# Optimization experiments

Measured on AMD Instinct MI355X. Metric: run time of the kernel, lower is better.

The kernel has to match this reference:

```python
import jax, jax.numpy as jnp
import numpy as np

S, B, D, Z, C, H = 256, 1024, 64, 32, 64, 128
L = 2 * S + 3  # len(ext_ts); _xs[0::2][1:-1] must match xs -> L = 2*S+3


def setup_inputs() -> dict:
    key = jax.random.key(0)
    ks = jax.random.split(key, 16)

    def xavier(k, out_d, in_d):
        lim = float(np.sqrt(6.0 / (in_d + out_d)))
        return jax.random.uniform(k, (out_d, in_d), minval=-lim, maxval=lim, dtype=jnp.float32)

    bias = lambda n: jnp.full((n,), 0.01, jnp.float32)  # m.bias.data.fill_(0.01)

    return {
        "xs": jax.random.normal(ks[0], (S, B, D), jnp.float32),
        "ext_ts": jnp.arange(L, dtype=jnp.float32) * 0.01,  # spacing <= dt=0.02 -> 1 euler step/interval
        "eps_z0": jax.random.normal(ks[1], (B, Z), jnp.float32),
        "dW": jax.random.normal(ks[2], (L - 1, B, Z), jnp.float32),  # standard normal; scaled by sqrt(dt) inside
        "gru_Wih": xavier(ks[3], 3 * H, D),
        "gru_Whh": xavier(ks[4], 3 * H, H),
        "gru_bih": jnp.zeros((3 * H,), jnp.float32),
        "gru_bhh": jnp.zeros((3 * H,), jnp.float32),
        "enc_W": xavier(ks[5], C, H), "enc_b": bias(C),
        "qz0_W": xavier(ks[6], 2 * Z, C), "qz0_b": bias(2 * Z),
        "f_W1": xavier(ks[7], H, Z + 1), "f_b1": bias(H),
        "f_W2": xavier(ks[8], H, H), "f_b2": bias(H),
        "f_W3": xavier(ks[9], Z, H), "f_b3": bias(Z),
        "g_W1": xavier(ks[10], H, Z + 1), "g_b1": bias(H),
        "g_W2": xavier(ks[11], Z, H), "g_b2": bias(Z),
        "proj_W": xavier(ks[12], D, Z), "proj_b": bias(D),
        "pz0_mean": jnp.zeros((1, Z), jnp.float32),
        "pz0_logstd": jnp.zeros((1, Z), jnp.float32),
    }


def reference(xs, ext_ts, eps_z0, dW, gru_Wih, gru_Whh, gru_bih, gru_bhh,
              enc_W, enc_b, qz0_W, qz0_b,
              f_W1, f_b1, f_W2, f_b2, f_W3, f_b3,
              g_W1, g_b1, g_W2, g_b2,
              proj_W, proj_b, pz0_mean, pz0_logstd):
    nb = xs.shape[1]
    # ---- Encoder: GRU over time-reversed xs; only ctx[0] (after flip-back) is
    # used, which equals lin(final hidden of the reversed-sequence GRU).
    x_rev = xs[::-1]
    gi_all = jnp.einsum('sbd,hd->sbh', x_rev, gru_Wih) + gru_bih  # (S,B,3H)

    def gru_step(h, gi_t):
        gh = h @ gru_Whh.T + gru_bhh
        i_r, i_z, i_n = jnp.split(gi_t, 3, axis=-1)
        h_r, h_z, h_n = jnp.split(gh, 3, axis=-1)
        r = jax.nn.sigmoid(i_r + h_r)
        zg = jax.nn.sigmoid(i_z + h_z)
        n = jnp.tanh(i_n + r * h_n)
        return (1.0 - zg) * n + zg * h, None

    hT, _ = jax.lax.scan(gru_step, jnp.zeros((nb, gru_Whh.shape[1]), xs.dtype), gi_all)
    ctx0 = hT @ enc_W.T + enc_b

    # ---- q(z0) and reparameterized sample
    q = ctx0 @ qz0_W.T + qz0_b
    qz0_mean, qz0_logstd = jnp.split(q, 2, axis=1)
    z0 = qz0_mean + jnp.exp(qz0_logstd) * eps_z0

    # ---- Euler-Maruyama SDE integration (diagonal noise), one step per interval
    dts = ext_ts[1:] - ext_ts[:-1]

    def sde_step(z, inp):
        t, dt, dw = inp
        tcol = jnp.broadcast_to(t.reshape(1, 1), (z.shape[0], 1)).astype(z.dtype)
        tz = jnp.concatenate([tcol, z], axis=1)  # (B, Z+1)
        h1 = jax.nn.relu(tz @ f_W1.T + f_b1)
        h2 = jax.nn.relu(h1 @ f_W2.T + f_b2)
        drift = h2 @ f_W3.T + f_b3
        gh = jax.nn.relu(tz @ g_W1.T + g_b1)
        diff = gh @ g_W2.T + g_b2
        z_new = z + drift * dt + diff * (jnp.sqrt(dt) * dw)
        return z_new, z_new

    _, zs_rest = jax.lax.scan(sde_step, z0, (ext_ts[:-1], dts, dW))
    zs = jnp.concatenate([z0[None], zs_rest], axis=0)  # (L,B,Z)

    # ---- project to data space and compute losses
    xs_hat = jnp.einsum('lbz,dz->lbd', zs, proj_W) + proj_b
    recon_xs = xs_hat[0::2][1:-1]   # (S,B,D)
    interp_xs = xs_hat[1::2][1:-1]  # (S-1,B,D)
    recon_loss = jnp.mean((recon_xs - xs) ** 2)

    # KL( N(qm, e^qls) || N(pm, e^pls) ), summed over latent, averaged over batch
    kl = (pz0_logstd - qz0_logstd
          + (jnp.exp(2.0 * qz0_logstd) + (qz0_mean - pz0_mean) ** 2)
          / (2.0 * jnp.exp(2.0 * pz0_logstd)) - 0.5)
    logqp0 = jnp.mean(jnp.sum(kl, axis=1))
    return recon_loss, logqp0, interp_xs
```

## Files before the change

### kernel.cpp

```cpp
#include <hip/hip_runtime.h>

typedef _Float16 f16;
typedef _Float16 h2 __attribute__((ext_vector_type(2)));
typedef _Float16 h8 __attribute__((ext_vector_type(8)));
typedef _Float16 v8h __attribute__((ext_vector_type(8)));
typedef _Float16 v4h __attribute__((ext_vector_type(4)));
typedef float    f4 __attribute__((ext_vector_type(4)));
typedef float    v4f __attribute__((ext_vector_type(4)));
typedef float    f2 __attribute__((ext_vector_type(2)));

#define S_  256
#define B_  1024
#define D_  64
#define H_  128
#define Z_  32
#define BD_ (B_*D_)
#define NSTEP 514

#define BAR() do { \
  asm volatile("s_waitcnt lgkmcnt(0)" ::: "memory"); \
  __builtin_amdgcn_s_barrier(); \
} while (0)

__device__ __forceinline__ h8 cvt8(f4 a, f4 b) {
  h8 w;
  w[0]=(f16)a[0]; w[1]=(f16)a[1]; w[2]=(f16)a[2]; w[3]=(f16)a[3];
  w[4]=(f16)b[0]; w[5]=(f16)b[1]; w[6]=(f16)b[2]; w[7]=(f16)b[3];
  return w;
}

__device__ __forceinline__ h8 ld8(const float* p) {
  f4 a = *(const f4*)p;
  f4 b = *(const f4*)(p + 4);
  return cvt8(a, b);
}

__device__ __forceinline__ float sigm(float x) { return 1.f / (1.f + __expf(-x)); }
__device__ __forceinline__ float tanh_(float x) {
  float e = __expf(-2.f * fabsf(x));
  float t = (1.f - e) / (1.f + e);
  return copysignf(t, x);
}

__global__ __launch_bounds__(256, 1) void gru_mfma_kernel(
    const float* __restrict__ xs, const float* __restrict__ Wih,
    const float* __restrict__ Whh, const float* __restrict__ bih,
    const float* __restrict__ bhh, float* __restrict__ hT)
{
  __shared__ f16 hB[2][16][136];

  const int t    = threadIdx.x;
  const int wid  = t >> 6;
  const int lane = t & 63;
  const int lr = lane & 15;
  const int lg = lane >> 4;
  const int r0 = blockIdx.x * 16;

  v8h whhR[2][4], whhZ[2][4], whhN[2][4];
  v8h wihR[2][2], wihZ[2][2], wihN[2][2];
  #pragma unroll
  for (int tt = 0; tt < 2; ++tt) {
    const int nr = wid*32 + tt*16 + lr;
    #pragma unroll
    for (int ks = 0; ks < 4; ++ks) {
      whhR[tt][ks] = ld8(Whh + (      nr)*H_ + ks*32 + lg*8);
      whhZ[tt][ks] = ld8(Whh + (128 + nr)*H_ + ks*32 + lg*8);
      whhN[tt][ks] = ld8(Whh + (256 + nr)*H_ + ks*32 + lg*8);
    }
    #pragma unroll
    for (int ks = 0; ks < 2; ++ks) {
      wihR[tt][ks] = ld8(Wih + (      nr)*D_ + ks*32 + lg*8);
      wihZ[tt][ks] = ld8(Wih + (128 + nr)*D_ + ks*32 + lg*8);
      wihN[tt][ks] = ld8(Wih + (256 + nr)*D_ + ks*32 + lg*8);
    }
  }
  v4f birh[2], bizh[2], binv[2], bhnv[2];
  #pragma unroll
  for (int tt = 0; tt < 2; ++tt) {
    const int nb = wid*32 + tt*16 + lg*4;
    v4f a = *(const v4f*)&bih[nb],     b = *(const v4f*)&bhh[nb];
    v4f c = *(const v4f*)&bih[128+nb], d = *(const v4f*)&bhh[128+nb];
    birh[tt] = a + b;
    bizh[tt] = c + d;
    binv[tt] = *(const v4f*)&bih[256+nb];
    bhnv[tt] = *(const v4f*)&bhh[256+nb];
  }

  for (int i = t; i < 16*136; i += 256) ((f16*)hB[0])[i] = (f16)0.f;
  v4f hm[2] = { {0.f,0.f,0.f,0.f}, {0.f,0.f,0.f,0.f} };
  const v4f zero4 = {0.f, 0.f, 0.f, 0.f};

  v8h bx0 = ld8(xs + (S_-1)*BD_ + (r0+lr)*D_ + lg*8);
  v8h bx1 = ld8(xs + (S_-1)*BD_ + (r0+lr)*D_ + 32 + lg*8);
  __syncthreads();

  int p = 0;
  #pragma unroll 1
  for (int s = 0; s < S_; ++s) {
    f4 ra0 = zero4, rb0 = zero4, ra1 = zero4, rb1 = zero4;
    const bool have = (s < S_-1);
    if (have) {
      const float* xp = xs + (S_-2-s)*BD_ + (r0+lr)*D_;
      ra0 = *(const f4*)(xp + lg*8);
      rb0 = *(const f4*)(xp + lg*8 + 4);
      ra1 = *(const f4*)(xp + 32 + lg*8);
      rb1 = *(const f4*)(xp + 32 + lg*8 + 4);
    }
    v8h bh[4];
    #pragma unroll
    for (int ks = 0; ks < 4; ++ks)
      bh[ks] = *(const v8h*)&hB[p][lr][ks*32 + lg*8];

    #pragma unroll
    for (int tt = 0; tt < 2; ++tt) {
      v4f ri  = __builtin_amdgcn_mfma_f32_16x16x32_f16(wihR[tt][0], bx0, zero4, 0,0,0);
      v4f zi  = __builtin_amdgcn_mfma_f32_16x16x32_f16(wihZ[tt][0], bx0, zero4, 0,0,0);
      v4f anx = __builtin_amdgcn_mfma_f32_16x16x32_f16(wihN[tt][0], bx0, zero4, 0,0,0);
      ri  = __builtin_amdgcn_mfma_f32_16x16x32_f16(wihR[tt][1], bx1, ri,  0,0,0);
      zi  = __builtin_amdgcn_mfma_f32_16x16x32_f16(wihZ[tt][1], bx1, zi,  0,0,0);
      anx = __builtin_amdgcn_mfma_f32_16x16x32_f16(wihN[tt][1], bx1, anx, 0,0,0);
      v4f rh = zero4, zh = zero4, anh = zero4;
      #pragma unroll
      for (int ks = 0; ks < 4; ++ks) {
        rh  = __builtin_amdgcn_mfma_f32_16x16x32_f16(whhR[tt][ks], bh[ks], rh,  0,0,0);
        zh  = __builtin_amdgcn_mfma_f32_16x16x32_f16(whhZ[tt][ks], bh[ks], zh,  0,0,0);
        anh = __builtin_amdgcn_mfma_f32_16x16x32_f16(whhN[tt][ks], bh[ks], anh, 0,0,0);
      }
      v4h o;
      #pragma unroll
      for (int i = 0; i < 4; ++i) {
        float r  = sigm(ri[i] + rh[i] + birh[tt][i]);
        float zg = sigm(zi[i] + zh[i] + bizh[tt][i]);
        float n  = tanh_(anx[i] + binv[tt][i] + r*(anh[i] + bhnv[tt][i]));
        hm[tt][i] = (1.f - zg)*n + zg*hm[tt][i];
        o[i] = (f16)hm[tt][i];
      }
      *(v4h*)&hB[p^1][lr][wid*32 + tt*16 + lg*4] = o;
    }
    BAR();
    if (have) { bx0 = cvt8(ra0, rb0); bx1 = cvt8(ra1, rb1); }
    p ^= 1;
  }

  #pragma unroll
  for (int tt = 0; tt < 2; ++tt)
    *(v4f*)&hT[(r0+lr)*H_ + wid*32 + tt*16 + lg*4] = hm[tt];
}

__global__ __launch_bounds__(256) void enc_kernel(
    const float* __restrict__ hT, const float* __restrict__ encW,
    const float* __restrict__ encB, const float* __restrict__ qW,
    const float* __restrict__ qB, const float* __restrict__ eps,
    const float* __restrict__ pm, const float* __restrict__ pls,
    float* __restrict__ z0, float* __restrict__ out)
{
  __shared__ float hTl[4][128];
  __shared__ float ctx[4][64];
  __shared__ float ql[4][64];
  const int t = threadIdx.x;
  const int b0 = blockIdx.x * 4;
  const int lb = t >> 6, j = t & 63;

  for (int i = t; i < 512; i += 256) hTl[i>>7][i&127] = hT[b0*H_ + i];
  __syncthreads();

  float acc = encB[j];
  #pragma unroll
  for (int k = 0; k < 128; k += 4) {
    f4 w = *(const f4*)&encW[j*128 + k];
    acc += hTl[lb][k]*w[0] + hTl[lb][k+1]*w[1] + hTl[lb][k+2]*w[2] + hTl[lb][k+3]*w[3];
  }
  ctx[lb][j] = acc;
  __syncthreads();

  float q = qB[j];
  #pragma unroll
  for (int k = 0; k < 64; k += 4) {
    f4 w = *(const f4*)&qW[j*64 + k];
    q += ctx[lb][k]*w[0] + ctx[lb][k+1]*w[1] + ctx[lb][k+2]*w[2] + ctx[lb][k+3]*w[3];
  }
  ql[lb][j] = q;
  __syncthreads();

  float kl = 0.f;
  if (j < 32) {
    float mean = ql[lb][j], ls = ql[lb][j+32];
    z0[(b0+lb)*Z_ + j] = mean + __expf(ls)*eps[(b0+lb)*Z_ + j];
    float pmj = pm[j], plsj = pls[j];
    float dm = mean - pmj;
    kl = plsj - ls + (__expf(2.f*ls) + dm*dm) / (2.f*__expf(2.f*plsj)) - 0.5f;
  }
  #pragma unroll
  for (int s2 = 32; s2 > 0; s2 >>= 1) kl += __shfl_down(kl, s2, 64);
  if (j == 0) atomicAdd(out + 1, kl * (1.f/1024.f));
}

__global__ __launch_bounds__(256, 1) void sde_mfma_kernel(
    const float* __restrict__ z0, const float* __restrict__ ts,
    const float* __restrict__ dW, const float* __restrict__ xs,
    const float* __restrict__ fW1, const float* __restrict__ fb1,
    const float* __restrict__ fW2, const float* __restrict__ fb2,
    const float* __restrict__ fW3, const float* __restrict__ fb3,
    const float* __restrict__ gW1, const float* __restrict__ gb1,
    const float* __restrict__ gW2, const float* __restrict__ gb2,
    const float* __restrict__ pW, const float* __restrict__ pb,
    float* __restrict__ out)
{
  __shared__ f16 Xa[16*72];
  __shared__ f16 h1A[16*168];
  __shared__ f16 ghA[16*168];
  __shared__ f16 h2A[16*168];
  __shared__ float tsL[516];
  __shared__ float lred[4];

  const int t    = threadIdx.x;
  const int wid  = t >> 6;
  const int lane = t & 63;
  const int lr = lane & 15;
  const int lg = lane >> 4;
  const int r0 = blockIdx.x * 16;
  const int wz = wid & 1;

  v8h w1r[8];
  #pragma unroll
  for (int nl = 0; nl < 4; ++nl) {
    const int n = wid*4 + nl;
    const float* src = (n < 8) ? (fW1 + (n*16+lr)*33) : (gW1 + ((n-8)*16+lr)*33);
    const float bsv  = (n < 8) ? fb1[n*16+lr] : gb1[(n-8)*16+lr];
    #pragma unroll
    for (int ks = 0; ks < 2; ++ks) {
      v8h w;
      #pragma unroll
      for (int j = 0; j < 8; ++j) {
        const int kp = ks*32 + lg*8 + j;
        float v;
        if (kp < 32)                   v = src[1+kp];
        else if (kp == 32 || kp == 34) v = src[0];
        else if (kp == 33)             v = bsv;
        else                           v = 0.f;
        w[j] = (f16)v;
      }
      w1r[nl*2+ks] = w;
    }
  }
  v8h w2r[10];
  #pragma unroll
  for (int nl = 0; nl < 2; ++nl) {
    const int n = wid*2 + nl;
    const float* src = fW2 + (n*16+lr)*128;
    const float bsv = fb2[n*16+lr];
    #pragma unroll
    for (int ks = 0; ks < 5; ++ks) {
      v8h w;
      #pragma unroll
      for (int j = 0; j < 8; ++j) {
        const int kp = ks*32 + lg*8 + j;
        float v = (kp < 128) ? src[kp] : ((kp == 128) ? bsv : 0.f);
        w[j] = (f16)v;
      }
      w2r[nl*5+ks] = w;
    }
  }
  v8h w3d[5], w3g[5];
  {
    const float* sd = fW3 + (wz*16+lr)*128;
    const float* sg = gW2 + (wz*16+lr)*128;
    const float bd = fb3[wz*16+lr], bg = gb2[wz*16+lr];
    #pragma unroll
    for (int ks = 0; ks < 5; ++ks) {
      v8h wd, wg;
      #pragma unroll
      for (int j = 0; j < 8; ++j) {
        const int kp = ks*32 + lg*8 + j;
        wd[j] = (f16)((kp < 128) ? sd[kp] : ((kp == 128) ? bd : 0.f));
        wg[j] = (f16)((kp < 128) ? sg[kp] : ((kp == 128) ? bg : 0.f));
      }
      w3d[ks] = wd; w3g[ks] = wg;
    }
  }
  v8h pwr[2];
  {
    const float* sp = pW + (wid*16+lr)*32;
    const float bp = pb[wid*16+lr];
    #pragma unroll
    for (int ks = 0; ks < 2; ++ks) {
      v8h w;
      #pragma unroll
      for (int j = 0; j < 8; ++j) {
        const int kp = ks*32 + lg*8 + j;
        w[j] = (f16)((kp < 32) ? sp[kp] : ((kp == 33) ? bp : 0.f));
      }
      pwr[ks] = w;
    }
  }

  for (int i = t; i < 16*72; i += 256) Xa[i] = (f16)0.f;
  for (int i = t; i < 16*168; i += 256) {
    h1A[i] = (f16)0.f; ghA[i] = (f16)0.f; h2A[i] = (f16)0.f;
  }
  for (int i = t; i < 515; i += 256) tsL[i] = ts[i];
  __syncthreads();
  if (t < 16) {
    Xa[t*72 + 33] = (f16)1.f;
    h1A[t*168 + 128] = (f16)1.f;
    ghA[t*168 + 128] = (f16)1.f;
    h2A[t*168 + 128] = (f16)1.f;
    const float t0 = tsL[0];
    const f16 th = (f16)t0;
    Xa[t*72 + 32] = th;
    Xa[t*72 + 34] = (f16)(t0 - (float)th);
  }
  const v4f zero4 = {0.f, 0.f, 0.f, 0.f};
  v4f zm = zero4;
  if (wid < 2) {
    zm = *(const v4f*)&z0[(r0+lr)*Z_ + wid*16 + lg*4];
    v4h a;
    #pragma unroll
    for (int i = 0; i < 4; ++i) a[i] = (f16)zm[i];
    *(v4h*)&Xa[lr*72 + wid*16 + lg*4] = a;
  }
  float loss = 0.f;
  bool pev = false, pod = false;
  int  pln = 0;
  v4f  pxv = zero4;
  __syncthreads();

  #pragma unroll 1
  for (int l = 0; l < NSTEP; ++l) {
    const float dt  = tsL[l+1] - tsL[l];
    const float sdt = sqrtf(dt);
    const int ln = l + 1;
    const bool ev = ((ln & 1) == 0) && ln >= 2 && ln <= 512;
    const bool od = ((ln & 1) == 1) && ln >= 3 && ln <= 511;

    v4f dwv = zero4;
    if (wid < 2) dwv = *(const v4f*)&dW[(l*B_ + r0 + lr)*Z_ + wid*16 + lg*4];
    v4f xvl = zero4;
    if (ev) xvl = *(const v4f*)&xs[(((ln-2)>>1)*B_ + r0 + lr)*D_ + wid*16 + lg*4];

    v4f pj = zero4;
    {
      const v8h bx0 = *(const v8h*)&Xa[lr*72 +  0 + lg*8];
      const v8h bx1 = *(const v8h*)&Xa[lr*72 + 32 + lg*8];
      #pragma unroll
      for (int nl = 0; nl < 4; ++nl) {
        v4f acc = __builtin_amdgcn_mfma_f32_16x16x32_f16(w1r[nl*2+0], bx0, zero4, 0, 0, 0);
        acc = __builtin_amdgcn_mfma_f32_16x16x32_f16(w1r[nl*2+1], bx1, acc, 0, 0, 0);
        v4h o;
        #pragma unroll
        for (int i = 0; i < 4; ++i) o[i] = (f16)fmaxf(acc[i], 0.f);
        if (wid < 2) *(v4h*)&h1A[lr*168 + (wid*4+nl)*16 + lg*4] = o;
        else         *(v4h*)&ghA[lr*168 + ((wid-2)*4+nl)*16 + lg*4] = o;
      }
      if (pev || pod) {
        pj = __builtin_amdgcn_mfma_f32_16x16x32_f16(pwr[0], bx0, zero4, 0, 0, 0);
        pj = __builtin_amdgcn_mfma_f32_16x16x32_f16(pwr[1], bx1, pj, 0, 0, 0);
      }
    }
    BAR();

    {
      v8h bh[5];
      #pragma unroll
      for (int ks = 0; ks < 5; ++ks) bh[ks] = *(const v8h*)&h1A[lr*168 + ks*32 + lg*8];
      v4f a0[2], a1[2];
      #pragma unroll
      for (int nl = 0; nl < 2; ++nl) {
        a0[nl] = __builtin_amdgcn_mfma_f32_16x16x32_f16(w2r[nl*5+0], bh[0], zero4, 0, 0, 0);
        a1[nl] = __builtin_amdgcn_mfma_f32_16x16x32_f16(w2r[nl*5+1], bh[1], zero4, 0, 0, 0);
        a0[nl] = __builtin_amdgcn_mfma_f32_16x16x32_f16(w2r[nl*5+2], bh[2], a0[nl], 0, 0, 0);
        a1[nl] = __builtin_amdgcn_mfma_f32_16x16x32_f16(w2r[nl*5+3], bh[3], a1[nl], 0, 0, 0);
        a0[nl] = __builtin_amdgcn_mfma_f32_16x16x32_f16(w2r[nl*5+4], bh[4], a0[nl], 0, 0, 0);
      }
      if (pev) {
        #pragma unroll
        for (int i = 0; i < 4; ++i) { float d = pj[i] - pxv[i]; loss = fmaf(d, d, loss); }
      } else if (pod) {
        float* op = out + 2 + (((pln-3)>>1)*B_ + r0 + lr)*D_ + wid*16 + lg*4;
        *(f2*)&op[0] = (f2){pj[0], pj[1]};
        *(f2*)&op[2] = (f2){pj[2], pj[3]};
      }
      #pragma unroll
      for (int nl = 0; nl < 2; ++nl) {
        v4f acc = a0[nl] + a1[nl];
        v4h o;
        #pragma unroll
        for (int i = 0; i < 4; ++i) o[i] = (f16)fmaxf(acc[i], 0.f);
        *(v4h*)&h2A[lr*168 + (wid*2+nl)*16 + lg*4] = o;
      }
    }
    BAR();

    if (wid < 2) {
      v4f d0 = zero4, d1 = zero4, f0 = zero4, f1 = zero4;
      v8h b2f[5], bgf[5];
      #pragma unroll
      for (int ks = 0; ks < 5; ++ks) {
        b2f[ks] = *(const v8h*)&h2A[lr*168 + ks*32 + lg*8];
        bgf[ks] = *(const v8h*)&ghA[lr*168 + ks*32 + lg*8];
      }
      d0 = __builtin_amdgcn_mfma_f32_16x16x32_f16(w3d[0], b2f[0], d0, 0, 0, 0);
      f0 = __builtin_amdgcn_mfma_f32_16x16x32_f16(w3g[0], bgf[0], f0, 0, 0, 0);
      d1 = __builtin_amdgcn_mfma_f32_16x16x32_f16(w3d[1], b2f[1], d1, 0, 0, 0);
      f1 = __builtin_amdgcn_mfma_f32_16x16x32_f16(w3g[1], bgf[1], f1, 0, 0, 0);
      d0 = __builtin_amdgcn_mfma_f32_16x16x32_f16(w3d[2], b2f[2], d0, 0, 0, 0);
      f0 = __builtin_amdgcn_mfma_f32_16x16x32_f16(w3g[2], bgf[2], f0, 0, 0, 0);
      d1 = __builtin_amdgcn_mfma_f32_16x16x32_f16(w3d[3], b2f[3], d1, 0, 0, 0);
      f1 = __builtin_amdgcn_mfma_f32_16x16x32_f16(w3g[3], bgf[3], f1, 0, 0, 0);
      d0 = __builtin_amdgcn_mfma_f32_16x16x32_f16(w3d[4], b2f[4], d0, 0, 0, 0);
      f0 = __builtin_amdgcn_mfma_f32_16x16x32_f16(w3g[4], bgf[4], f0, 0, 0, 0);
      #pragma unroll
      for (int i = 0; i < 4; ++i)
        zm[i] += (d0[i] + d1[i])*dt + (f0[i] + f1[i])*(sdt*dwv[i]);
      v4h a;
      #pragma unroll
      for (int i = 0; i < 4; ++i) a[i] = (f16)zm[i];
      *(v4h*)&Xa[lr*72 + wid*16 + lg*4] = a;
    } else if (wid == 3 && lg == 0) {
      const float tn = tsL[l+1];
      const f16 th = (f16)tn;
      Xa[lr*72 + 32] = th;
      Xa[lr*72 + 34] = (f16)(tn - (float)th);
    }
    BAR();

    pev = ev; pod = od; pln = ln;
    if (ev) pxv = xvl;
  }

  #pragma unroll
  for (int s2 = 32; s2 > 0; s2 >>= 1) loss += __shfl_down(loss, s2, 64);
  if (lane == 0) lred[wid] = loss;
  __syncthreads();
  if (t == 0)
    atomicAdd(out + 0, (lred[0] + lred[1] + lred[2] + lred[3]) * (1.f/16777216.f));
}

extern "C" void kernel_launch(void* const* d_in, const int* in_sizes, int n_in,
                              void* d_out, int out_size, void* d_ws, size_t ws_size,
                              hipStream_t stream) {
  (void)in_sizes; (void)n_in; (void)out_size; (void)ws_size;
  const float* xs   = (const float*)d_in[0];
  const float* ts   = (const float*)d_in[1];
  const float* eps  = (const float*)d_in[2];
  const float* dWp  = (const float*)d_in[3];
  const float* Wih  = (const float*)d_in[4];
  const float* Whh  = (const float*)d_in[5];
  const float* bih  = (const float*)d_in[6];
  const float* bhh  = (const float*)d_in[7];
  const float* encW = (const float*)d_in[8];
  const float* encB = (const float*)d_in[9];
  const float* qW   = (const float*)d_in[10];
  const float* qB   = (const float*)d_in[11];
  const float* fW1  = (const float*)d_in[12];
  const float* fb1  = (const float*)d_in[13];
  const float* fW2  = (const float*)d_in[14];
  const float* fb2  = (const float*)d_in[15];
  const float* fW3  = (const float*)d_in[16];
  const float* fb3  = (const float*)d_in[17];
  const float* gW1  = (const float*)d_in[18];
  const float* gb1  = (const float*)d_in[19];
  const float* gW2  = (const float*)d_in[20];
  const float* gb2  = (const float*)d_in[21];
  const float* pW   = (const float*)d_in[22];
  const float* pb   = (const float*)d_in[23];
  const float* pm   = (const float*)d_in[24];
  const float* pls  = (const float*)d_in[25];

  float* out = (float*)d_out;
  float* ws  = (float*)d_ws;
  float* hT = ws;
  float* z0 = ws + 131072;

  hipMemsetAsync(d_out, 0, 2*sizeof(float), stream);
  hipLaunchKernelGGL(gru_mfma_kernel, dim3(64), dim3(256), 0, stream,
                     xs, Wih, Whh, bih, bhh, hT);
  hipLaunchKernelGGL(enc_kernel, dim3(256), dim3(256), 0, stream,
                     hT, encW, encB, qW, qB, eps, pm, pls, z0, out);
  hipLaunchKernelGGL(sde_mfma_kernel, dim3(64), dim3(256), 0, stream,
                     z0, ts, dWp, xs, fW1, fb1, fW2, fb2, fW3, fb3,
                     gW1, gb1, gW2, gb2, pW, pb, out);
}
```

Before: 1.064 ms.

## Process two 16-row batch tiles per block in GRU and SDE kernels

Each block of the GRU and SDE recurrence kernels now handles 32 batch rows as two 16-row sub-tiles, and the grid is halved from 64 to 32 blocks. The register-resident weights are reused across both sub-tiles, and the independent MFMA chains of the two tiles can interleave to hide latency within each serial step. In the SDE final stage all four waves now do work (two per sub-tile) instead of two sitting idle. The cost is that only half as many CUs are used and each step's critical path is longer, so it relies on the sequential recurrence being latency-bound rather than throughput-bound.

```diff
diff --git a/kernel.cpp b/kernel.cpp
--- a/kernel.cpp
+++ b/kernel.cpp
@@ -47,14 +47,14 @@
     const float* __restrict__ Whh, const float* __restrict__ bih,
     const float* __restrict__ bhh, float* __restrict__ hT)
 {
-  __shared__ f16 hB[2][16][136];
+  __shared__ f16 hB[2][2][16][136];
 
   const int t    = threadIdx.x;
   const int wid  = t >> 6;
   const int lane = t & 63;
   const int lr = lane & 15;
   const int lg = lane >> 4;
-  const int r0 = blockIdx.x * 16;
+  const int r0 = blockIdx.x * 32;
 
   v8h whhR[2][4], whhZ[2][4], whhN[2][4];
   v8h wihR[2][2], wihZ[2][2], wihN[2][2];
@@ -86,65 +86,87 @@
     bhnv[tt] = *(const v4f*)&bhh[256+nb];
   }
 
-  for (int i = t; i < 16*136; i += 256) ((f16*)hB[0])[i] = (f16)0.f;
-  v4f hm[2] = { {0.f,0.f,0.f,0.f}, {0.f,0.f,0.f,0.f} };
+  for (int i = t; i < 2*16*136; i += 256) ((f16*)hB[0])[i] = (f16)0.f;
+  v4f hm[2][2] = { { {0.f,0.f,0.f,0.f}, {0.f,0.f,0.f,0.f} },
+                   { {0.f,0.f,0.f,0.f}, {0.f,0.f,0.f,0.f} } };
   const v4f zero4 = {0.f, 0.f, 0.f, 0.f};
 
-  v8h bx0 = ld8(xs + (S_-1)*BD_ + (r0+lr)*D_ + lg*8);
-  v8h bx1 = ld8(xs + (S_-1)*BD_ + (r0+lr)*D_ + 32 + lg*8);
+  v8h bx0[2], bx1[2];
+  #pragma unroll
+  for (int u = 0; u < 2; ++u) {
+    bx0[u] = ld8(xs + (S_-1)*BD_ + (r0+u*16+lr)*D_ + lg*8);
+    bx1[u] = ld8(xs + (S_-1)*BD_ + (r0+u*16+lr)*D_ + 32 + lg*8);
+  }
   __syncthreads();
 
   int p = 0;
   #pragma unroll 1
   for (int s = 0; s < S_; ++s) {
-    f4 ra0 = zero4, rb0 = zero4, ra1 = zero4, rb1 = zero4;
+    f4 ra0[2], rb0[2], ra1[2], rb1[2];
     const bool have = (s < S_-1);
+    #pragma unroll
+    for (int u = 0; u < 2; ++u) {
+      ra0[u] = zero4; rb0[u] = zero4; ra1[u] = zero4; rb1[u] = zero4;
+      if (have) {
+        const float* xp = xs + (S_-2-s)*BD_ + (r0+u*16+lr)*D_;
+        ra0[u] = *(const f4*)(xp + lg*8);
+        rb0[u] = *(const f4*)(xp + lg*8 + 4);
+        ra1[u] = *(const f4*)(xp + 32 + lg*8);
+        rb1[u] = *(const f4*)(xp + 32 + lg*8 + 4);
+      }
+    }
+    v8h bh[2][4];
+    #pragma unroll
+    for (int u = 0; u < 2; ++u)
+      #pragma unroll
+      for (int ks = 0; ks < 4; ++ks)
+        bh[u][ks] = *(const v8h*)&hB[p][u][lr][ks*32 + lg*8];
+
+    #pragma unroll
+    for (int tt = 0; tt < 2; ++tt) {
+      #pragma unroll
+      for (int u = 0; u < 2; ++u) {
+        v4f ri  = __builtin_amdgcn_mfma_f32_16x16x32_f16(wihR[tt][0], bx0[u], zero4, 0,0,0);
+        v4f zi  = __builtin_amdgcn_mfma_f32_16x16x32_f16(wihZ[tt][0], bx0[u], zero4, 0,0,0);
+        v4f anx = __builtin_amdgcn_mfma_f32_16x16x32_f16(wihN[tt][0], bx0[u], zero4, 0,0,0);
+        ri  = __builtin_amdgcn_mfma_f32_16x16x32_f16(wihR[tt][1], bx1[u], ri,  0,0,0);
+        zi  = __builtin_amdgcn_mfma_f32_16x16x32_f16(wihZ[tt][1], bx1[u], zi,  0,0,0);
+        anx = __builtin_amdgcn_mfma_f32_16x16x32_f16(wihN[tt][1], bx1[u], anx, 0,0,0);
+        v4f rh = zero4, zh = zero4, anh = zero4;
+        #pragma unroll
+        for (int ks = 0; ks < 4; ++ks) {
+          rh  = __builtin_amdgcn_mfma_f32_16x16x32_f16(whhR[tt][ks], bh[u][ks], rh,  0,0,0);
+          zh  = __builtin_amdgcn_mfma_f32_16x16x32_f16(whhZ[tt][ks], bh[u][ks], zh,  0,0,0);
+          anh = __builtin_amdgcn_mfma_f32_16x16x32_f16(whhN[tt][ks], bh[u][ks], anh, 0,0,0);
+        }
+        v4h o;
+        #pragma unroll
+        for (int i = 0; i < 4; ++i) {
+          float r  = sigm(ri[i] + rh[i] + birh[tt][i]);
+          float zg = sigm(zi[i] + zh[i] + bizh[tt][i]);
+          float n  = tanh_(anx[i] + binv[tt][i] + r*(anh[i] + bhnv[tt][i]));
+          hm[u][tt][i] = (1.f - zg)*n + zg*hm[u][tt][i];
+          o[i] = (f16)hm[u][tt][i];
+        }
+        *(v4h*)&hB[p^1][u][lr][wid*32 + tt*16 + lg*4] = o;
+      }
+    }
+    BAR();
     if (have) {
-      const float* xp = xs + (S_-2-s)*BD_ + (r0+lr)*D_;
-      ra0 = *(const f4*)(xp + lg*8);
-      rb0 = *(const f4*)(xp + lg*8 + 4);
-      ra1 = *(const f4*)(xp + 32 + lg*8);
-      rb1 = *(const f4*)(xp + 32 + lg*8 + 4);
-    }
-    v8h bh[4];
-    #pragma unroll
-    for (int ks = 0; ks < 4; ++ks)
-      bh[ks] = *(const v8h*)&hB[p][lr][ks*32 + lg*8];
-
-    #pragma unroll
-    for (int tt = 0; tt < 2; ++tt) {
-      v4f ri  = __builtin_amdgcn_mfma_f32_16x16x32_f16(wihR[tt][0], bx0, zero4, 0,0,0);
-      v4f zi  = __builtin_amdgcn_mfma_f32_16x16x32_f16(wihZ[tt][0], bx0, zero4, 0,0,0);
-      v4f anx = __builtin_amdgcn_mfma_f32_16x16x32_f16(wihN[tt][0], bx0, zero4, 0,0,0);
-      ri  = __builtin_amdgcn_mfma_f32_16x16x32_f16(wihR[tt][1], bx1, ri,  0,0,0);
-      zi  = __builtin_amdgcn_mfma_f32_16x16x32_f16(wihZ[tt][1], bx1, zi,  0,0,0);
-      anx = __builtin_amdgcn_mfma_f32_16x16x32_f16(wihN[tt][1], bx1, anx, 0,0,0);
-      v4f rh = zero4, zh = zero4, anh = zero4;
-      #pragma unroll
-      for (int ks = 0; ks < 4; ++ks) {
-        rh  = __builtin_amdgcn_mfma_f32_16x16x32_f16(whhR[tt][ks], bh[ks], rh,  0,0,0);
-        zh  = __builtin_amdgcn_mfma_f32_16x16x32_f16(whhZ[tt][ks], bh[ks], zh,  0,0,0);
-        anh = __builtin_amdgcn_mfma_f32_16x16x32_f16(whhN[tt][ks], bh[ks], anh, 0,0,0);
-      }
-      v4h o;
-      #pragma unroll
-      for (int i = 0; i < 4; ++i) {
-        float r  = sigm(ri[i] + rh[i] + birh[tt][i]);
-        float zg = sigm(zi[i] + zh[i] + bizh[tt][i]);
-        float n  = tanh_(anx[i] + binv[tt][i] + r*(anh[i] + bhnv[tt][i]));
-        hm[tt][i] = (1.f - zg)*n + zg*hm[tt][i];
-        o[i] = (f16)hm[tt][i];
-      }
-      *(v4h*)&hB[p^1][lr][wid*32 + tt*16 + lg*4] = o;
-    }
-    BAR();
-    if (have) { bx0 = cvt8(ra0, rb0); bx1 = cvt8(ra1, rb1); }
+      #pragma unroll
+      for (int u = 0; u < 2; ++u) {
+        bx0[u] = cvt8(ra0[u], rb0[u]);
+        bx1[u] = cvt8(ra1[u], rb1[u]);
+      }
+    }
     p ^= 1;
   }
 
   #pragma unroll
-  for (int tt = 0; tt < 2; ++tt)
-    *(v4f*)&hT[(r0+lr)*H_ + wid*32 + tt*16 + lg*4] = hm[tt];
+  for (int u = 0; u < 2; ++u)
+    #pragma unroll
+    for (int tt = 0; tt < 2; ++tt)
+      *(v4f*)&hT[(r0+u*16+lr)*H_ + wid*32 + tt*16 + lg*4] = hm[u][tt];
 }
 
 __global__ __launch_bounds__(256) void enc_kernel(
@@ -206,10 +228,10 @@
     const float* __restrict__ pW, const float* __restrict__ pb,
     float* __restrict__ out)
 {
-  __shared__ f16 Xa[16*72];
-  __shared__ f16 h1A[16*168];
-  __shared__ f16 ghA[16*168];
-  __shared__ f16 h2A[16*168];
+  __shared__ f16 Xa[2][16*72];
+  __shared__ f16 h1A[2][16*168];
+  __shared__ f16 ghA[2][16*168];
+  __shared__ f16 h2A[2][16*168];
   __shared__ float tsL[516];
   __shared__ float lred[4];
 
@@ -218,8 +240,9 @@
   const int lane = t & 63;
   const int lr = lane & 15;
   const int lg = lane >> 4;
-  const int r0 = blockIdx.x * 16;
+  const int r0 = blockIdx.x * 32;
   const int wz = wid & 1;
+  const int tw = wid >> 1;
 
   v8h w1r[8];
   #pragma unroll
@@ -294,35 +317,39 @@
     }
   }
 
-  for (int i = t; i < 16*72; i += 256) Xa[i] = (f16)0.f;
-  for (int i = t; i < 16*168; i += 256) {
-    h1A[i] = (f16)0.f; ghA[i] = (f16)0.f; h2A[i] = (f16)0.f;
+  for (int i = t; i < 2*16*72; i += 256) ((f16*)Xa[0])[i] = (f16)0.f;
+  for (int i = t; i < 2*16*168; i += 256) {
+    ((f16*)h1A[0])[i] = (f16)0.f;
+    ((f16*)ghA[0])[i] = (f16)0.f;
+    ((f16*)h2A[0])[i] = (f16)0.f;
   }
   for (int i = t; i < 515; i += 256) tsL[i] = ts[i];
   __syncthreads();
   if (t < 16) {
-    Xa[t*72 + 33] = (f16)1.f;
-    h1A[t*168 + 128] = (f16)1.f;
-    ghA[t*168 + 128] = (f16)1.f;
-    h2A[t*168 + 128] = (f16)1.f;
-    const float t0 = tsL[0];
-    const f16 th = (f16)t0;
-    Xa[t*72 + 32] = th;
-    Xa[t*72 + 34] = (f16)(t0 - (float)th);
+    const float t0v = tsL[0];
+    const f16 th0 = (f16)t0v;
+    #pragma unroll
+    for (int u = 0; u < 2; ++u) {
+      Xa[u][t*72 + 33] = (f16)1.f;
+      h1A[u][t*168 + 128] = (f16)1.f;
+      ghA[u][t*168 + 128] = (f16)1.f;
+      h2A[u][t*168 + 128] = (f16)1.f;
+      Xa[u][t*72 + 32] = th0;
+      Xa[u][t*72 + 34] = (f16)(t0v - (float)th0);
+    }
   }
   const v4f zero4 = {0.f, 0.f, 0.f, 0.f};
-  v4f zm = zero4;
-  if (wid < 2) {
-    zm = *(const v4f*)&z0[(r0+lr)*Z_ + wid*16 + lg*4];
+  v4f zm = *(const v4f*)&z0[(r0 + tw*16 + lr)*Z_ + wz*16 + lg*4];
+  {
     v4h a;
     #pragma unroll
     for (int i = 0; i < 4; ++i) a[i] = (f16)zm[i];
-    *(v4h*)&Xa[lr*72 + wid*16 + lg*4] = a;
+    *(v4h*)&Xa[tw][lr*72 + wz*16 + lg*4] = a;
   }
   float loss = 0.f;
   bool pev = false, pod = false;
   int  pln = 0;
-  v4f  pxv = zero4;
+  v4f  pxv[2] = {zero4, zero4};
   __syncthreads();
 
   #pragma unroll 1
@@ -333,72 +360,99 @@
     const bool ev = ((ln & 1) == 0) && ln >= 2 && ln <= 512;
     const bool od = ((ln & 1) == 1) && ln >= 3 && ln <= 511;
 
-    v4f dwv = zero4;
-    if (wid < 2) dwv = *(const v4f*)&dW[(l*B_ + r0 + lr)*Z_ + wid*16 + lg*4];
-    v4f xvl = zero4;
-    if (ev) xvl = *(const v4f*)&xs[(((ln-2)>>1)*B_ + r0 + lr)*D_ + wid*16 + lg*4];
-
-    v4f pj = zero4;
+    v4f dwv = *(const v4f*)&dW[(l*B_ + r0 + tw*16 + lr)*Z_ + wz*16 + lg*4];
+    v4f xvl[2] = {zero4, zero4};
+    if (ev) {
+      #pragma unroll
+      for (int u = 0; u < 2; ++u)
+        xvl[u] = *(const v4f*)&xs[(((ln-2)>>1)*B_ + r0 + u*16 + lr)*D_ + wid*16 + lg*4];
+    }
+
+    v4f pj[2] = {zero4, zero4};
     {
-      const v8h bx0 = *(const v8h*)&Xa[lr*72 +  0 + lg*8];
-      const v8h bx1 = *(const v8h*)&Xa[lr*72 + 32 + lg*8];
+      v8h bx0[2], bx1[2];
+      #pragma unroll
+      for (int u = 0; u < 2; ++u) {
+        bx0[u] = *(const v8h*)&Xa[u][lr*72 +  0 + lg*8];
+        bx1[u] = *(const v8h*)&Xa[u][lr*72 + 32 + lg*8];
+      }
       #pragma unroll
       for (int nl = 0; nl < 4; ++nl) {
-        v4f acc = __builtin_amdgcn_mfma_f32_16x16x32_f16(w1r[nl*2+0], bx0, zero4, 0, 0, 0);
-        acc = __builtin_amdgcn_mfma_f32_16x16x32_f16(w1r[nl*2+1], bx1, acc, 0, 0, 0);
-        v4h o;
-        #pragma unroll
-        for (int i = 0; i < 4; ++i) o[i] = (f16)fmaxf(acc[i], 0.f);
-        if (wid < 2) *(v4h*)&h1A[lr*168 + (wid*4+nl)*16 + lg*4] = o;
-        else         *(v4h*)&ghA[lr*168 + ((wid-2)*4+nl)*16 + lg*4] = o;
+        #pragma unroll
+        for (int u = 0; u < 2; ++u) {
+          v4f acc = __builtin_amdgcn_mfma_f32_16x16x32_f16(w1r[nl*2+0], bx0[u], zero4, 0, 0, 0);
+          acc = __builtin_amdgcn_mfma_f32_16x16x32_f16(w1r[nl*2+1], bx1[u], acc, 0, 0, 0);
+          v4h o;
+          #pragma unroll
+          for (int i = 0; i < 4; ++i) o[i] = (f16)fmaxf(acc[i], 0.f);
+          if (wid < 2) *(v4h*)&h1A[u][lr*168 + (wid*4+nl)*16 + lg*4] = o;
+          else         *(v4h*)&ghA[u][lr*168 + ((wid-2)*4+nl)*16 + lg*4] = o;
+        }
       }
       if (pev || pod) {
-        pj = __builtin_amdgcn_mfma_f32_16x16x32_f16(pwr[0], bx0, zero4, 0, 0, 0);
-        pj = __builtin_amdgcn_mfma_f32_16x16x32_f16(pwr[1], bx1, pj, 0, 0, 0);
+        #pragma unroll
+        for (int u = 0; u < 2; ++u) {
+          pj[u] = __builtin_amdgcn_mfma_f32_16x16x32_f16(pwr[0], bx0[u], zero4, 0, 0, 0);
+          pj[u] = __builtin_amdgcn_mfma_f32_16x16x32_f16(pwr[1], bx1[u], pj[u], 0, 0, 0);
+        }
       }
     }
     BAR();
 
     {
-      v8h bh[5];
-      #pragma unroll
-      for (int ks = 0; ks < 5; ++ks) bh[ks] = *(const v8h*)&h1A[lr*168 + ks*32 + lg*8];
-      v4f a0[2], a1[2];
+      v8h bh[2][5];
+      #pragma unroll
+      for (int u = 0; u < 2; ++u)
+        #pragma unroll
+        for (int ks = 0; ks < 5; ++ks)
+          bh[u][ks] = *(const v8h*)&h1A[u][lr*168 + ks*32 + lg*8];
+      v4f a0[2][2], a1[2][2];
       #pragma unroll
       for (int nl = 0; nl < 2; ++nl) {
-        a0[nl] = __builtin_amdgcn_mfma_f32_16x16x32_f16(w2r[nl*5+0], bh[0], zero4, 0, 0, 0);
-        a1[nl] = __builtin_amdgcn_mfma_f32_16x16x32_f16(w2r[nl*5+1], bh[1], zero4, 0, 0, 0);
-        a0[nl] = __builtin_amdgcn_mfma_f32_16x16x32_f16(w2r[nl*5+2], bh[2], a0[nl], 0, 0, 0);
-        a1[nl] = __builtin_amdgcn_mfma_f32_16x16x32_f16(w2r[nl*5+3], bh[3], a1[nl], 0, 0, 0);
-        a0[nl] = __builtin_amdgcn_mfma_f32_16x16x32_f16(w2r[nl*5+4], bh[4], a0[nl], 0, 0, 0);
+        #pragma unroll
+        for (int u = 0; u < 2; ++u) {
+          a0[u][nl] = __builtin_amdgcn_mfma_f32_16x16x32_f16(w2r[nl*5+0], bh[u][0], zero4, 0, 0, 0);
+          a1[u][nl] = __builtin_amdgcn_mfma_f32_16x16x32_f16(w2r[nl*5+1], bh[u][1], zero4, 0, 0, 0);
+          a0[u][nl] = __builtin_amdgcn_mfma_f32_16x16x32_f16(w2r[nl*5+2], bh[u][2], a0[u][nl], 0, 0, 0);
+          a1[u][nl] = __builtin_amdgcn_mfma_f32_16x16x32_f16(w2r[nl*5+3], bh[u][3], a1[u][nl], 0, 0, 0);
+          a0[u][nl] = __builtin_amdgcn_mfma_f32_16x16x32_f16(w2r[nl*5+4], bh[u][4], a0[u][nl], 0, 0, 0);
+        }
       }
       if (pev) {
         #pragma unroll
-        for (int i = 0; i < 4; ++i) { float d = pj[i] - pxv[i]; loss = fmaf(d, d, loss); }
+        for (int u = 0; u < 2; ++u)
+          #pragma unroll
+          for (int i = 0; i < 4; ++i) { float d = pj[u][i] - pxv[u][i]; loss = fmaf(d, d, loss); }
       } else if (pod) {
-        float* op = out + 2 + (((pln-3)>>1)*B_ + r0 + lr)*D_ + wid*16 + lg*4;
-        *(f2*)&op[0] = (f2){pj[0], pj[1]};
-        *(f2*)&op[2] = (f2){pj[2], pj[3]};
+        #pragma unroll
+        for (int u = 0; u < 2; ++u) {
+          float* op = out + 2 + (((pln-3)>>1)*B_ + r0 + u*16 + lr)*D_ + wid*16 + lg*4;
+          *(f2*)&op[0] = (f2){pj[u][0], pj[u][1]};
+          *(f2*)&op[2] = (f2){pj[u][2], pj[u][3]};
+        }
       }
       #pragma unroll
       for (int nl = 0; nl < 2; ++nl) {
-        v4f acc = a0[nl] + a1[nl];
-        v4h o;
-        #pragma unroll
-        for (int i = 0; i < 4; ++i) o[i] = (f16)fmaxf(acc[i], 0.f);
-        *(v4h*)&h2A[lr*168 + (wid*2+nl)*16 + lg*4] = o;
+        #pragma unroll
+        for (int u = 0; u < 2; ++u) {
+          v4f acc = a0[u][nl] + a1[u][nl];
+          v4h o;
+          #pragma unroll
+          for (int i = 0; i < 4; ++i) o[i] = (f16)fmaxf(acc[i], 0.f);
+          *(v4h*)&h2A[u][lr*168 + (wid*2+nl)*16 + lg*4] = o;
+        }
       }
     }
     BAR();
 
-    if (wid < 2) {
+    {
+      v8h b2f[5], bgf[5];
+      #pragma unroll
+      for (int ks = 0; ks < 5; ++ks) {
+        b2f[ks] = *(const v8h*)&h2A[tw][lr*168 + ks*32 + lg*8];
+        bgf[ks] = *(const v8h*)&ghA[tw][lr*168 + ks*32 + lg*8];
+      }
       v4f d0 = zero4, d1 = zero4, f0 = zero4, f1 = zero4;
-      v8h b2f[5], bgf[5];
-      #pragma unroll
-      for (int ks = 0; ks < 5; ++ks) {
-        b2f[ks] = *(const v8h*)&h2A[lr*168 + ks*32 + lg*8];
-        bgf[ks] = *(const v8h*)&ghA[lr*168 + ks*32 + lg*8];
-      }
       d0 = __builtin_amdgcn_mfma_f32_16x16x32_f16(w3d[0], b2f[0], d0, 0, 0, 0);
       f0 = __builtin_amdgcn_mfma_f32_16x16x32_f16(w3g[0], bgf[0], f0, 0, 0, 0);
       d1 = __builtin_amdgcn_mfma_f32_16x16x32_f16(w3d[1], b2f[1], d1, 0, 0, 0);
@@ -415,17 +469,18 @@
       v4h a;
       #pragma unroll
       for (int i = 0; i < 4; ++i) a[i] = (f16)zm[i];
-      *(v4h*)&Xa[lr*72 + wid*16 + lg*4] = a;
-    } else if (wid == 3 && lg == 0) {
-      const float tn = tsL[l+1];
-      const f16 th = (f16)tn;
-      Xa[lr*72 + 32] = th;
-      Xa[lr*72 + 34] = (f16)(tn - (float)th);
+      *(v4h*)&Xa[tw][lr*72 + wz*16 + lg*4] = a;
+      if (wz == 0 && lg == 0) {
+        const float tn = tsL[l+1];
+        const f16 th = (f16)tn;
+        Xa[tw][lr*72 + 32] = th;
+        Xa[tw][lr*72 + 34] = (f16)(tn - (float)th);
+      }
     }
     BAR();
 
     pev = ev; pod = od; pln = ln;
-    if (ev) pxv = xvl;
+    if (ev) { pxv[0] = xvl[0]; pxv[1] = xvl[1]; }
   }
 
   #pragma unroll
@@ -473,11 +528,11 @@
   float* z0 = ws + 131072;
 
   hipMemsetAsync(d_out, 0, 2*sizeof(float), stream);
-  hipLaunchKernelGGL(gru_mfma_kernel, dim3(64), dim3(256), 0, stream,
+  hipLaunchKernelGGL(gru_mfma_kernel, dim3(32), dim3(256), 0, stream,
                      xs, Wih, Whh, bih, bhh, hT);
   hipLaunchKernelGGL(enc_kernel, dim3(256), dim3(256), 0, stream,
                      hT, encW, encB, qW, qB, eps, pm, pls, z0, out);
-  hipLaunchKernelGGL(sde_mfma_kernel, dim3(64), dim3(256), 0, stream,
+  hipLaunchKernelGGL(sde_mfma_kernel, dim3(32), dim3(256), 0, stream,
                      z0, ts, dWp, xs, fW1, fb1, fW2, fb2, fW3, fb3,
                      gW1, gb1, gW2, gb2, pW, pb, out);
 }
```

New measurement: 1.648 ms. 1.55x slower.
